# Kernel tuning notes

Measured on AMD Instinct MI355X. Metric: run time of the kernel, lower is better.

The kernel has to match this reference:

```python
import jax, jax.numpy as jnp
import numpy as np

B, N, NPOINT, NSAMPLE, CIN = 8, 16384, 2048, 32, 64
MLP = (64, 64, 128)
EPS = 1e-5  # torch BatchNorm2d default eps


def setup_inputs() -> dict:
    key = jax.random.key(0)
    ks = jax.random.split(key, 8)
    xyz = jax.random.normal(ks[0], (B, 3, N), dtype=jnp.float32)
    points = jax.random.normal(ks[1], (B, CIN, N), dtype=jnp.float32)
    # torch.randperm(N)[:npoint], shared across batch
    sample_idx = jax.random.permutation(ks[2], N)[:NPOINT].astype(jnp.int32)
    c0 = CIN + 3
    def conv_w(k, o, i):
        return jax.random.normal(k, (o, i), dtype=jnp.float32) * np.float32(1.0 / np.sqrt(i))
    W1 = conv_w(ks[3], MLP[0], c0)
    W2 = conv_w(ks[4], MLP[1], MLP[0])
    W3 = conv_w(ks[5], MLP[2], MLP[1])
    return {
        "xyz": xyz, "points": points, "sample_idx": sample_idx,
        "W1": W1, "b1": jnp.zeros((MLP[0],), jnp.float32), "g1": jnp.ones((MLP[0],), jnp.float32), "be1": jnp.zeros((MLP[0],), jnp.float32),
        "W2": W2, "b2": jnp.zeros((MLP[1],), jnp.float32), "g2": jnp.ones((MLP[1],), jnp.float32), "be2": jnp.zeros((MLP[1],), jnp.float32),
        "W3": W3, "b3": jnp.zeros((MLP[2],), jnp.float32), "g3": jnp.ones((MLP[2],), jnp.float32), "be3": jnp.zeros((MLP[2],), jnp.float32),
    }


def _bn(h, g, b):
    # training-mode BatchNorm2d: per-channel (last axis) stats over all other dims, biased var
    m = jnp.mean(h, axis=(0, 1, 2), keepdims=True)
    v = jnp.mean(jnp.square(h - m), axis=(0, 1, 2), keepdims=True)
    return (h - m) * jax.lax.rsqrt(v + EPS) * g + b


def reference(xyz, points, sample_idx, W1, b1, g1, be1, W2, b2, g2, be2, W3, b3, g3, be3):
    # sample npoint centroids (shared indices across batch, as in the torch code)
    q = jnp.take(xyz, sample_idx, axis=2).transpose(0, 2, 1)   # (B, npoint, 3)
    p = xyz.transpose(0, 2, 1)                                  # (B, N, 3)
    # squared pairwise distances (same ordering as cdist for topk)
    d2 = (jnp.sum(q * q, -1)[:, :, None]
          + jnp.sum(p * p, -1)[:, None, :]
          - 2.0 * jnp.einsum('bqc,bnc->bqn', q, p))             # (B, npoint, N)
    _, idx = jax.lax.top_k(-d2, NSAMPLE)                        # (B, npoint, nsample) smallest dists

    gxyz = jnp.take_along_axis(p[:, None, :, :], idx[:, :, :, None], axis=2)  # (B, npoint, nsample, 3)
    rel = gxyz - q[:, :, None, :]
    pf = points.transpose(0, 2, 1)                              # (B, N, C)
    gpts = jnp.take_along_axis(pf[:, None, :, :], idx[:, :, :, None], axis=2)  # (B, npoint, nsample, C)
    feat = jnp.concatenate([rel, gpts], axis=-1)                # (B, npoint, nsample, 3+C)

    h = jax.nn.relu(_bn(jnp.einsum('bpsc,oc->bpso', feat, W1) + b1, g1, be1))
    h = jax.nn.relu(_bn(jnp.einsum('bpsc,oc->bpso', h, W2) + b2, g2, be2))
    h = _bn(jnp.einsum('bpsc,oc->bpso', h, W3) + b3, g3, be3)
    new_points = jnp.max(h, axis=2)                             # max over nsample -> (B, npoint, mlp2)
    return q.transpose(0, 2, 1), new_points.transpose(0, 2, 1)  # (B,3,npoint), (B,mlp2,npoint)
```

## Files before the change

kernel.cpp:

```cpp
#include <hip/hip_runtime.h>
#include <cstdint>

#define DEVFN __device__ __forceinline__

constexpr int B_ = 8, N_ = 16384, NP_ = 2048, NS_ = 32;
constexpr int S_ = B_ * NP_ * NS_;
constexpr float INV_CNT = 1.0f / 524288.0f;

typedef __attribute__((ext_vector_type(8))) short bf8_t;
typedef __attribute__((ext_vector_type(4))) float f4_t;
#define MFMA16(A, Bv, C) __builtin_amdgcn_mfma_f32_16x16x32_bf16(A, Bv, C, 0, 0, 0)

DEVFN unsigned long long wredmin64(unsigned long long v) {
  for (int o = 32; o; o >>= 1) { unsigned long long u = __shfl_xor(v, o); v = u < v ? u : v; }
  return v;
}
DEVFN float d2_ref(float4 q, float4 p) {
  float dot = __fadd_rn(__fadd_rn(__fmul_rn(q.x, p.x), __fmul_rn(q.y, p.y)), __fmul_rn(q.z, p.z));
  return __fsub_rn(__fadd_rn(q.w, p.w), __fadd_rn(dot, dot));
}
DEVFN unsigned int fmono(float d) {
  unsigned int u = __float_as_uint(d);
  return u ^ ((u >> 31) ? 0xFFFFFFFFu : 0x80000000u);
}
DEVFN unsigned short f2bf(float f) {
  unsigned int u = __float_as_uint(f);
  u += 0x7FFFu + ((u >> 16) & 1u);
  return (unsigned short)(u >> 16);
}
DEVFN bf8_t ld_bf8(const unsigned short* p) {
  union { uint4 u; bf8_t b; } cv;
  cv.u = *reinterpret_cast<const uint4*>(p);
  return cv.b;
}

__global__ __launch_bounds__(256) void prep_xyzw(const float* __restrict__ xyz, float4* __restrict__ xyzw) {
  int t = blockIdx.x * 256 + threadIdx.x;
  int b = t >> 14, n = t & (N_ - 1);
  const float* X = xyz + (size_t)b * 3 * N_;
  float x = X[n], y = X[N_ + n], z = X[2 * N_ + n];
  float sq = __fadd_rn(__fadd_rn(__fmul_rn(x, x), __fmul_rn(y, y)), __fmul_rn(z, z));
  xyzw[t] = make_float4(x, y, z, sq);
}

__global__ __launch_bounds__(256) void prep_q(const int* __restrict__ sidx, const float4* __restrict__ xyzw,
                                              float4* __restrict__ qw, float* __restrict__ out_q) {
  int t = blockIdx.x * 256 + threadIdx.x;
  int b = t >> 11, p = t & (NP_ - 1);
  int n = sidx[p] & (N_ - 1);
  float4 v = xyzw[b * N_ + n];
  qw[t] = v;
  out_q[((size_t)b * 3 + 0) * NP_ + p] = v.x;
  out_q[((size_t)b * 3 + 1) * NP_ + p] = v.y;
  out_q[((size_t)b * 3 + 2) * NP_ + p] = v.z;
}

__global__ __launch_bounds__(256) void transpose_bf16(const float* __restrict__ in, unsigned short* __restrict__ out) {
  __shared__ float tile[32][33];
  int b = blockIdx.x >> 10;
  int rem = blockIdx.x & 1023;
  int c0 = (rem >> 9) << 5;
  int n0 = (rem & 511) << 5;
  int tx = threadIdx.x & 31, ty = threadIdx.x >> 5;
#pragma unroll
  for (int jj = 0; jj < 4; jj++) {
    int c = c0 + ty + jj * 8;
    tile[ty + jj * 8][tx] = in[((size_t)b * 64 + c) * N_ + n0 + tx];
  }
  __syncthreads();
#pragma unroll
  for (int jj = 0; jj < 4; jj++) {
    int n = n0 + ty + jj * 8;
    out[((size_t)b * N_ + n) * 64 + c0 + tx] = f2bf(tile[tx][ty + jj * 8]);
  }
}

__global__ __launch_bounds__(256) void prep_w(const float* __restrict__ W1, const float* __restrict__ W2,
                                              const float* __restrict__ W3, unsigned short* __restrict__ W1b,
                                              unsigned short* __restrict__ W2b, unsigned short* __restrict__ W3b) {
  int t = blockIdx.x * 256 + threadIdx.x;
  int stride = gridDim.x * 256;
  for (int e = t; e < 64 * 96; e += stride) {
    int o = e / 96, k = e - o * 96;
    float v = (k < 64) ? W1[o * 67 + 3 + k] : (k < 67 ? W1[o * 67 + (k - 64)] : 0.0f);
    W1b[e] = f2bf(v);
  }
  for (int e = t; e < 64 * 64; e += stride) W2b[e] = f2bf(W2[e]);
  for (int e = t; e < 128 * 64; e += stride) W3b[e] = f2bf(W3[e]);
}

__global__ __launch_bounds__(256) void knn_kernel(const float4* __restrict__ xyzw, const float4* __restrict__ qw,
                                                  int* __restrict__ idx_out) {
  __shared__ unsigned short surv[32][256];
  __shared__ float4 Pst[1024];
  int tid = threadIdx.x;
  int wave = tid >> 6, lane = tid & 63;
  int b = blockIdx.x >> 6;
  int q0 = (blockIdx.x & 63) * 32 + wave * 8;
  const float4* P = xyzw + b * N_;
  float4 Q[8];
#pragma unroll
  for (int j = 0; j < 8; j++) Q[j] = qw[b * NP_ + q0 + j];

  float dmin[8];
#pragma unroll
  for (int j = 0; j < 8; j++) dmin[j] = 1e30f;
  for (int c = 0; c < N_ / 1024; c++) {
    __syncthreads();
#pragma unroll
    for (int u = 0; u < 4; u++) Pst[tid + u * 256] = P[c * 1024 + tid + u * 256];
    __syncthreads();
#pragma unroll 1
    for (int t = 0; t < 16; t++) {
      float4 p = Pst[t * 64 + lane];
      float kx = -2.0f * p.x, ky = -2.0f * p.y, kz = -2.0f * p.z;
#pragma unroll
      for (int j = 0; j < 8; j++) {
        float key = __fmaf_rn(kx, Q[j].x, __fmaf_rn(ky, Q[j].y, __fmaf_rn(kz, Q[j].z, p.w)));
        dmin[j] = fminf(dmin[j], key);
      }
    }
  }
  float T[8];
#pragma unroll 1
  for (int j = 0; j < 8; j++) {
    float v = dmin[j];
#pragma unroll
    for (int k = 2; k <= 64; k <<= 1)
#pragma unroll
      for (int s = k >> 1; s > 0; s >>= 1) {
        float o = __shfl_xor(v, s);
        bool up = ((lane & k) == 0);
        bool tmin = (((lane & s) == 0) == up);
        v = tmin ? fminf(v, o) : fmaxf(v, o);
      }
    T[j] = __shfl(v, 31);
  }
  int base[8];
#pragma unroll
  for (int j = 0; j < 8; j++) base[j] = 0;
  for (int c = 0; c < N_ / 1024; c++) {
    __syncthreads();
#pragma unroll
    for (int u = 0; u < 4; u++) Pst[tid + u * 256] = P[c * 1024 + tid + u * 256];
    __syncthreads();
#pragma unroll 1
    for (int t = 0; t < 16; t++) {
      float4 p = Pst[t * 64 + lane];
      float kx = -2.0f * p.x, ky = -2.0f * p.y, kz = -2.0f * p.z;
#pragma unroll
      for (int j = 0; j < 8; j++) {
        float key = __fmaf_rn(kx, Q[j].x, __fmaf_rn(ky, Q[j].y, __fmaf_rn(kz, Q[j].z, p.w)));
        bool pred = key <= T[j];
        unsigned long long mask = __ballot(pred);
        if (mask) {
          if (pred) {
            int off = base[j] + __popcll(mask & ((1ull << lane) - 1ull));
            if (off < 256) surv[wave * 8 + j][off] = (unsigned short)(c * 1024 + t * 64 + lane);
          }
          base[j] += __popcll(mask);
        }
      }
    }
  }
#pragma unroll 1
  for (int j = 0; j < 8; j++) {
    int qq = wave * 8 + j;
    int m = base[j] < 256 ? base[j] : 256;
    if (m <= 64) {
      unsigned long long v = ~0ull;
      if (lane < m) {
        int n = surv[qq][lane];
        float4 p = P[n];
        float d2 = d2_ref(Q[j], p);
        v = ((unsigned long long)fmono(d2) << 32) | (unsigned int)n;
      }
#pragma unroll
      for (int k = 2; k <= 64; k <<= 1)
#pragma unroll
        for (int s = k >> 1; s > 0; s >>= 1) {
          unsigned long long o = __shfl_xor(v, s);
          bool up = ((lane & k) == 0);
          bool tmin = (((lane & s) == 0) == up);
          unsigned long long lo = v < o ? v : o;
          unsigned long long hi = v < o ? o : v;
          v = tmin ? lo : hi;
        }
      if (lane < 32) idx_out[(b * NP_ + q0 + j) * NS_ + lane] = (int)(v & 0xFFFFu);
    } else {
      unsigned long long k4[4];
#pragma unroll
      for (int t = 0; t < 4; t++) {
        int ii = t * 64 + lane;
        k4[t] = ~0ull;
        if (ii < m) {
          int n = surv[qq][ii];
          float4 p = P[n];
          float d2 = d2_ref(Q[j], p);
          k4[t] = ((unsigned long long)fmono(d2) << 32) | (unsigned int)n;
        }
      }
      int keep = 0;
      for (int r = 0; r < 32; r++) {
        unsigned long long loc = k4[0];
        loc = k4[1] < loc ? k4[1] : loc;
        loc = k4[2] < loc ? k4[2] : loc;
        loc = k4[3] < loc ? k4[3] : loc;
        unsigned long long km = wredmin64(loc);
#pragma unroll
        for (int t = 0; t < 4; t++) if (k4[t] == km) k4[t] = ~0ull;
        if (lane == r) keep = (int)(km & 0xFFFFu);
      }
      if (lane < 32) idx_out[(b * NP_ + q0 + j) * NS_ + lane] = keep;
    }
  }
}

template <int STAGES>
__global__ __launch_bounds__(256, (STAGES == 1) ? 4 : 3) void fused_kernel(
    const int* __restrict__ idx, const float4* __restrict__ xyzw, const float4* __restrict__ qw,
    const unsigned short* __restrict__ pTb, const unsigned short* __restrict__ W1b,
    const unsigned short* __restrict__ W2b, const unsigned short* __restrict__ W3b,
    const float* __restrict__ b1, const float* __restrict__ g1, const float* __restrict__ be1,
    const float* __restrict__ stats1,
    const float* __restrict__ b2, const float* __restrict__ g2, const float* __restrict__ be2,
    const float* __restrict__ stats2,
    const float* __restrict__ b3,
    float* __restrict__ statsOut, float* __restrict__ maxmin) {
  __shared__ unsigned short W1L[64 * 104];
  __shared__ unsigned short W2L[(STAGES >= 2) ? 64 * 72 : 8];
  __shared__ unsigned short W3L[(STAGES == 3) ? 128 * 72 : 8];
  __shared__ unsigned short hbuf[(STAGES >= 2) ? 64 * 64 : 8];
  __shared__ float smx[(STAGES == 3) ? 4 : 1][128];
  __shared__ float smn[(STAGES == 3) ? 4 : 1][128];
  __shared__ float sAcc[256];
  constexpr int NJL = (STAGES == 3) ? 8 : 4;

  int tid = threadIdx.x;
  int w = tid >> 6, l = tid & 63;
  int c16 = l & 15, g = l >> 4;

  for (int e = tid; e < 64 * 12; e += 256) {
    int r = e / 12, c = e % 12;
    *(uint4*)&W1L[r * 104 + c * 8] = *(const uint4*)&W1b[r * 96 + c * 8];
  }
  if (STAGES >= 2)
    for (int e = tid; e < 64 * 8; e += 256) {
      int r = e >> 3, c = e & 7;
      *(uint4*)&W2L[r * 72 + c * 8] = *(const uint4*)&W2b[r * 64 + c * 8];
    }
  if (STAGES == 3)
    for (int e = tid; e < 128 * 8; e += 256) {
      int r = e >> 3, c = e & 7;
      *(uint4*)&W3L[r * 72 + c * 8] = *(const uint4*)&W3b[r * 64 + c * 8];
    }

  float rb1[4], ra1[4], rd1[4], rb2[4], ra2[4], rd2[4], rb3[8];
#pragma unroll
  for (int j = 0; j < 4; j++) rb1[j] = b1[j * 16 + c16];
  if (STAGES >= 2) {
#pragma unroll
    for (int j = 0; j < 4; j++) {
      int ch = j * 16 + c16;
      float m = stats1[ch] * INV_CNT;
      float v = stats1[64 + ch] * INV_CNT - m * m;
      float a = rsqrtf(v + 1e-5f) * g1[ch];
      ra1[j] = a; rd1[j] = be1[ch] - m * a;
      rb2[j] = b2[ch];
    }
  }
  if (STAGES == 3) {
#pragma unroll
    for (int j = 0; j < 4; j++) {
      int ch = j * 16 + c16;
      float m = stats2[ch] * INV_CNT;
      float v = stats2[64 + ch] * INV_CNT - m * m;
      float a = rsqrtf(v + 1e-5f) * g2[ch];
      ra2[j] = a; rd2[j] = be2[ch] - m * a;
    }
#pragma unroll
    for (int j = 0; j < 8; j++) rb3[j] = b3[j * 16 + c16];
  }

  float st1[NJL], st2[NJL];
#pragma unroll
  for (int j = 0; j < NJL; j++) { st1[j] = 0.0f; st2[j] = 0.0f; }

  __syncthreads();

  for (int tile = blockIdx.x; tile < S_ / 64; tile += gridDim.x) {
    int b = tile >> 10;
    int s = tile * 64 + w * 16 + c16;
    int n = idx[s] & (N_ - 1);
    const unsigned short* arow = pTb + (((size_t)(b << 14) + n) << 6);
    bf8_t a0 = ld_bf8(arow + g * 8);
    bf8_t a1 = ld_bf8(arow + 32 + g * 8);
    float4 P = xyzw[(b << 14) + n];
    float4 Q = qw[tile * 2 + (w >> 1)];
    bf8_t a2 = {0, 0, 0, 0, 0, 0, 0, 0};
    if (g == 0) {
      a2[0] = (short)f2bf(P.x - Q.x);
      a2[1] = (short)f2bf(P.y - Q.y);
      a2[2] = (short)f2bf(P.z - Q.z);
    }
    f4_t acc1[4];
#pragma unroll
    for (int j = 0; j < 4; j++) {
      bf8_t w0 = ld_bf8(&W1L[(j * 16 + c16) * 104 + 0 * 32 + g * 8]);
      bf8_t w1 = ld_bf8(&W1L[(j * 16 + c16) * 104 + 1 * 32 + g * 8]);
      bf8_t w2 = ld_bf8(&W1L[(j * 16 + c16) * 104 + 2 * 32 + g * 8]);
      acc1[j] = (f4_t){0.0f, 0.0f, 0.0f, 0.0f};
      acc1[j] = MFMA16(a0, w0, acc1[j]);
      acc1[j] = MFMA16(a1, w1, acc1[j]);
      acc1[j] = MFMA16(a2, w2, acc1[j]);
    }
    if (STAGES == 1) {
#pragma unroll
      for (int j = 0; j < 4; j++)
#pragma unroll
        for (int r = 0; r < 4; r++) {
          float h = acc1[j][r] + rb1[j];
          st1[j] += h; st2[j] += h * h;
        }
      continue;
    }
    if (STAGES == 2) __syncthreads();
#pragma unroll
    for (int j = 0; j < 4; j++)
#pragma unroll
      for (int r = 0; r < 4; r++) {
        float h = acc1[j][r] + rb1[j];
        float t = fmaxf(0.0f, fmaf(h, ra1[j], rd1[j]));
        int row = w * 16 + g * 4 + r, ch = j * 16 + c16;
        hbuf[row * 64 + (((ch >> 3) ^ (row & 7)) << 3) + (ch & 7)] = f2bf(t);
      }
    __syncthreads();
    int rrow = w * 16 + c16;
    bf8_t h1f[2];
#pragma unroll
    for (int kb = 0; kb < 2; kb++)
      h1f[kb] = ld_bf8(hbuf + rrow * 64 + (((kb * 4 + g) ^ (rrow & 7)) << 3));
    f4_t acc2[4];
#pragma unroll
    for (int j = 0; j < 4; j++) {
      bf8_t w0 = ld_bf8(&W2L[(j * 16 + c16) * 72 + g * 8]);
      bf8_t w1 = ld_bf8(&W2L[(j * 16 + c16) * 72 + 32 + g * 8]);
      acc2[j] = (f4_t){0.0f, 0.0f, 0.0f, 0.0f};
      acc2[j] = MFMA16(h1f[0], w0, acc2[j]);
      acc2[j] = MFMA16(h1f[1], w1, acc2[j]);
    }
    if (STAGES == 2) {
#pragma unroll
      for (int j = 0; j < 4; j++)
#pragma unroll
        for (int r = 0; r < 4; r++) {
          float h = acc2[j][r] + rb2[j];
          st1[j] += h; st2[j] += h * h;
        }
      continue;
    }
    __syncthreads();
#pragma unroll
    for (int j = 0; j < 4; j++)
#pragma unroll
      for (int r = 0; r < 4; r++) {
        float h = acc2[j][r] + rb2[j];
        float t = fmaxf(0.0f, fmaf(h, ra2[j], rd2[j]));
        int row = w * 16 + g * 4 + r, ch = j * 16 + c16;
        hbuf[row * 64 + (((ch >> 3) ^ (row & 7)) << 3) + (ch & 7)] = f2bf(t);
      }
    __syncthreads();
    bf8_t h2f[2];
#pragma unroll
    for (int kb = 0; kb < 2; kb++)
      h2f[kb] = ld_bf8(hbuf + rrow * 64 + (((kb * 4 + g) ^ (rrow & 7)) << 3));
    f4_t acc3[8];
#pragma unroll
    for (int j = 0; j < 8; j++) {
      bf8_t w0 = ld_bf8(&W3L[(j * 16 + c16) * 72 + g * 8]);
      bf8_t w1 = ld_bf8(&W3L[(j * 16 + c16) * 72 + 32 + g * 8]);
      acc3[j] = (f4_t){0.0f, 0.0f, 0.0f, 0.0f};
      acc3[j] = MFMA16(h2f[0], w0, acc3[j]);
      acc3[j] = MFMA16(h2f[1], w1, acc3[j]);
    }
    float mx[8], mn[8];
#pragma unroll
    for (int j = 0; j < 8; j++) {
      mx[j] = -1e30f; mn[j] = 1e30f;
#pragma unroll
      for (int r = 0; r < 4; r++) {
        float h = acc3[j][r] + rb3[j];
        st1[j] += h; st2[j] += h * h;
        mx[j] = fmaxf(mx[j], h); mn[j] = fminf(mn[j], h);
      }
      mx[j] = fmaxf(mx[j], __shfl_xor(mx[j], 16));
      mx[j] = fmaxf(mx[j], __shfl_xor(mx[j], 32));
      mn[j] = fminf(mn[j], __shfl_xor(mn[j], 16));
      mn[j] = fminf(mn[j], __shfl_xor(mn[j], 32));
    }
    if (l < 16) {
#pragma unroll
      for (int j = 0; j < 8; j++) { smx[w][j * 16 + l] = mx[j]; smn[w][j * 16 + l] = mn[j]; }
    }
    __syncthreads();
    {
      int cen = tid >> 7, ch = tid & 127;
      float vx = fmaxf(smx[2 * cen][ch], smx[2 * cen + 1][ch]);
      float vn = fminf(smn[2 * cen][ch], smn[2 * cen + 1][ch]);
      size_t gcen = (size_t)tile * 2 + cen;
      maxmin[gcen * 256 + ch * 2 + 0] = vx;
      maxmin[gcen * 256 + ch * 2 + 1] = vn;
    }
  }
  __syncthreads();
  if (tid < 2 * NJL * 16) sAcc[tid] = 0.0f;
  __syncthreads();
#pragma unroll
  for (int j = 0; j < NJL; j++) {
    atomicAdd(&sAcc[j * 16 + c16], st1[j]);
    atomicAdd(&sAcc[NJL * 16 + j * 16 + c16], st2[j]);
  }
  __syncthreads();
  if (tid < 2 * NJL * 16) atomicAdd(&statsOut[tid], sAcc[tid]);
}

__global__ __launch_bounds__(256) void finalize_kernel(const float* __restrict__ maxmin,
                                                       const float* __restrict__ stats3,
                                                       const float* __restrict__ g3, const float* __restrict__ be3,
                                                       float* __restrict__ out_np) {
  int o = blockIdx.x * 256 + threadIdx.x;
  int p = o & 2047, ch = (o >> 11) & 127, b = o >> 18;
  float m = stats3[ch] * INV_CNT;
  float v = stats3[128 + ch] * INV_CNT - m * m;
  float a = rsqrtf(v + 1e-5f) * g3[ch];
  float d = be3[ch] - m * a;
  size_t g = (size_t)(b * 2048 + p);
  float hi = maxmin[g * 256 + ch * 2 + 0];
  float lo = maxmin[g * 256 + ch * 2 + 1];
  out_np[o] = fmaf(a, (a >= 0.0f ? hi : lo), d);
}

extern "C" void kernel_launch(void* const* d_in, const int* in_sizes, int n_in,
                              void* d_out, int out_size, void* d_ws, size_t ws_size,
                              hipStream_t stream) {
  const float* xyz = (const float*)d_in[0];
  const float* points = (const float*)d_in[1];
  const int* sidx = (const int*)d_in[2];
  const float* W1 = (const float*)d_in[3];
  const float* b1 = (const float*)d_in[4];
  const float* g1 = (const float*)d_in[5];
  const float* be1 = (const float*)d_in[6];
  const float* W2 = (const float*)d_in[7];
  const float* b2 = (const float*)d_in[8];
  const float* g2 = (const float*)d_in[9];
  const float* be2 = (const float*)d_in[10];
  const float* W3 = (const float*)d_in[11];
  const float* b3 = (const float*)d_in[12];
  const float* g3 = (const float*)d_in[13];
  const float* be3 = (const float*)d_in[14];

  float* out_q = (float*)d_out;
  float* out_np = (float*)d_out + (size_t)B_ * 3 * NP_;

  char* ws = (char*)d_ws;
  float* stats1 = (float*)(ws + 0);
  float* stats2 = (float*)(ws + 512);
  float* stats3 = (float*)(ws + 1024);
  size_t off = 4096;
  float4* xyzw = (float4*)(ws + off); off += (size_t)B_ * N_ * 16;
  float4* qw = (float4*)(ws + off);   off += (size_t)B_ * NP_ * 16;
  int* idxb = (int*)(ws + off);       off += (size_t)B_ * NP_ * NS_ * 4;
  unsigned short* pTb = (unsigned short*)(ws + off); off += (size_t)B_ * N_ * 64 * 2;
  unsigned short* W1b = (unsigned short*)(ws + off); off += 64 * 96 * 2;
  unsigned short* W2b = (unsigned short*)(ws + off); off += 64 * 64 * 2;
  unsigned short* W3b = (unsigned short*)(ws + off); off += 128 * 64 * 2;
  float* maxmin = (float*)(ws + off);  off += (size_t)B_ * NP_ * 128 * 2 * 4;

  hipMemsetAsync(ws, 0, 4096, stream);
  prep_xyzw<<<B_ * N_ / 256, 256, 0, stream>>>(xyz, xyzw);
  prep_q<<<B_ * NP_ / 256, 256, 0, stream>>>(sidx, xyzw, qw, out_q);
  transpose_bf16<<<B_ * 2 * (N_ / 32), 256, 0, stream>>>(points, pTb);
  prep_w<<<72, 256, 0, stream>>>(W1, W2, W3, W1b, W2b, W3b);
  knn_kernel<<<B_ * (NP_ / 32), 256, 0, stream>>>(xyzw, qw, idxb);
  fused_kernel<1><<<1024, 256, 0, stream>>>(idxb, xyzw, qw, pTb, W1b, W2b, W3b,
      b1, g1, be1, stats1, b2, g2, be2, stats2, b3, stats1, maxmin);
  fused_kernel<2><<<1024, 256, 0, stream>>>(idxb, xyzw, qw, pTb, W1b, W2b, W3b,
      b1, g1, be1, stats1, b2, g2, be2, stats2, b3, stats2, maxmin);
  fused_kernel<3><<<1024, 256, 0, stream>>>(idxb, xyzw, qw, pTb, W1b, W2b, W3b,
      b1, g1, be1, stats1, b2, g2, be2, stats2, b3, stats3, maxmin);
  finalize_kernel<<<(B_ * 128 * NP_) / 256, 256, 0, stream>>>(maxmin, stats3, g3, be3, out_np);
}
```

Before: 483.8 us.

## Materialize MLP activations in bf16 and restructure kNN to split points across waves

The recompute scheme, where each BN stage re-runs every earlier layer, is replaced by three kernels that write pre-BN activations as bf16 to a workspace buffer and read them back for the next layer. BN and ReLU are applied when the data is loaded. This trades about 64 MB of global traffic per stage for the repeated layer-1/layer-2 matmuls and gathers. The kNN kernel now gives each block 16 queries, with each wave scanning a quarter of the points for all 16 queries. Survivor counts are merged through shared-memory atomics, which adds atomic and sync overhead but reduces the per-wave point loop. The new path runs only when the workspace is large enough, and the old path stays as a fallback.

```diff
diff --git a/kernel.cpp b/kernel.cpp
--- a/kernel.cpp
+++ b/kernel.cpp
@@ -10,6 +10,8 @@
 typedef __attribute__((ext_vector_type(8))) short bf8_t;
 typedef __attribute__((ext_vector_type(4))) float f4_t;
 #define MFMA16(A, Bv, C) __builtin_amdgcn_mfma_f32_16x16x32_bf16(A, Bv, C, 0, 0, 0)
+
+union u4s8 { uint4 u; unsigned short s[8]; };
 
 DEVFN unsigned long long wredmin64(unsigned long long v) {
   for (int o = 32; o; o >>= 1) { unsigned long long u = __shfl_xor(v, o); v = u < v ? u : v; }
@@ -89,42 +91,53 @@
   for (int e = t; e < 128 * 64; e += stride) W3b[e] = f2bf(W3[e]);
 }
 
-__global__ __launch_bounds__(256) void knn_kernel(const float4* __restrict__ xyzw, const float4* __restrict__ qw,
-                                                  int* __restrict__ idx_out) {
-  __shared__ unsigned short surv[32][256];
+__global__ __launch_bounds__(256, 4) void knn_kernel(const float4* __restrict__ xyzw,
+                                                     const float4* __restrict__ qw,
+                                                     int* __restrict__ idx_out) {
   __shared__ float4 Pst[1024];
-  int tid = threadIdx.x;
-  int wave = tid >> 6, lane = tid & 63;
-  int b = blockIdx.x >> 6;
-  int q0 = (blockIdx.x & 63) * 32 + wave * 8;
+  __shared__ unsigned short surv[16][256];
+  __shared__ float Tsh[16];
+  __shared__ int cnt[16];
+  int tid = threadIdx.x, wave = tid >> 6, lane = tid & 63;
+  int b = blockIdx.x >> 7;
+  int q0 = (blockIdx.x & 127) * 16;
   const float4* P = xyzw + b * N_;
-  float4 Q[8];
-#pragma unroll
-  for (int j = 0; j < 8; j++) Q[j] = qw[b * NP_ + q0 + j];
-
-  float dmin[8];
-#pragma unroll
-  for (int j = 0; j < 8; j++) dmin[j] = 1e30f;
+  float Qx[16], Qy[16], Qz[16];
+#pragma unroll
+  for (int j = 0; j < 16; j++) {
+    float4 q = qw[b * NP_ + q0 + j];
+    Qx[j] = q.x; Qy[j] = q.y; Qz[j] = q.z;
+  }
+  float dmin[16];
+#pragma unroll
+  for (int j = 0; j < 16; j++) dmin[j] = 1e30f;
   for (int c = 0; c < N_ / 1024; c++) {
     __syncthreads();
 #pragma unroll
     for (int u = 0; u < 4; u++) Pst[tid + u * 256] = P[c * 1024 + tid + u * 256];
     __syncthreads();
+#pragma unroll
+    for (int t = 0; t < 4; t++) {
+      float4 p = Pst[wave * 256 + t * 64 + lane];
+      float kx = -2.0f * p.x, ky = -2.0f * p.y, kz = -2.0f * p.z;
+#pragma unroll
+      for (int j = 0; j < 16; j++) {
+        float key = __fmaf_rn(kx, Qx[j], __fmaf_rn(ky, Qy[j], __fmaf_rn(kz, Qz[j], p.w)));
+        dmin[j] = fminf(dmin[j], key);
+      }
+    }
+  }
+  __syncthreads();
+  float* dl = (float*)Pst;
+#pragma unroll
+  for (int j = 0; j < 16; j++) dl[j * 256 + wave * 64 + lane] = dmin[j];
+  if (tid < 16) cnt[tid] = 0;
+  __syncthreads();
 #pragma unroll 1
-    for (int t = 0; t < 16; t++) {
-      float4 p = Pst[t * 64 + lane];
-      float kx = -2.0f * p.x, ky = -2.0f * p.y, kz = -2.0f * p.z;
-#pragma unroll
-      for (int j = 0; j < 8; j++) {
-        float key = __fmaf_rn(kx, Q[j].x, __fmaf_rn(ky, Q[j].y, __fmaf_rn(kz, Q[j].z, p.w)));
-        dmin[j] = fminf(dmin[j], key);
-      }
-    }
-  }
-  float T[8];
-#pragma unroll 1
-  for (int j = 0; j < 8; j++) {
-    float v = dmin[j];
+  for (int jj = 0; jj < 4; jj++) {
+    int j = wave * 4 + jj;
+    float v = fminf(fminf(dl[j * 256 + lane], dl[j * 256 + 64 + lane]),
+                    fminf(dl[j * 256 + 128 + lane], dl[j * 256 + 192 + lane]));
 #pragma unroll
     for (int k = 2; k <= 64; k <<= 1)
 #pragma unroll
@@ -134,45 +147,51 @@
         bool tmin = (((lane & s) == 0) == up);
         v = tmin ? fminf(v, o) : fmaxf(v, o);
       }
-    T[j] = __shfl(v, 31);
-  }
-  int base[8];
-#pragma unroll
-  for (int j = 0; j < 8; j++) base[j] = 0;
+    if (lane == 31) Tsh[j] = v;
+  }
+  __syncthreads();
+  float T[16];
+#pragma unroll
+  for (int j = 0; j < 16; j++) T[j] = Tsh[j];
   for (int c = 0; c < N_ / 1024; c++) {
     __syncthreads();
 #pragma unroll
     for (int u = 0; u < 4; u++) Pst[tid + u * 256] = P[c * 1024 + tid + u * 256];
     __syncthreads();
 #pragma unroll 1
-    for (int t = 0; t < 16; t++) {
-      float4 p = Pst[t * 64 + lane];
+    for (int t = 0; t < 4; t++) {
+      int n = c * 1024 + wave * 256 + t * 64 + lane;
+      float4 p = Pst[wave * 256 + t * 64 + lane];
       float kx = -2.0f * p.x, ky = -2.0f * p.y, kz = -2.0f * p.z;
 #pragma unroll
-      for (int j = 0; j < 8; j++) {
-        float key = __fmaf_rn(kx, Q[j].x, __fmaf_rn(ky, Q[j].y, __fmaf_rn(kz, Q[j].z, p.w)));
+      for (int j = 0; j < 16; j++) {
+        float key = __fmaf_rn(kx, Qx[j], __fmaf_rn(ky, Qy[j], __fmaf_rn(kz, Qz[j], p.w)));
         bool pred = key <= T[j];
         unsigned long long mask = __ballot(pred);
         if (mask) {
+          int basew;
+          if (lane == 0) basew = atomicAdd(&cnt[j], (int)__popcll(mask));
+          basew = __shfl(basew, 0);
           if (pred) {
-            int off = base[j] + __popcll(mask & ((1ull << lane) - 1ull));
-            if (off < 256) surv[wave * 8 + j][off] = (unsigned short)(c * 1024 + t * 64 + lane);
+            int off = basew + (int)__popcll(mask & ((1ull << lane) - 1ull));
+            if (off < 256) surv[j][off] = (unsigned short)n;
           }
-          base[j] += __popcll(mask);
         }
       }
     }
   }
+  __syncthreads();
 #pragma unroll 1
-  for (int j = 0; j < 8; j++) {
-    int qq = wave * 8 + j;
-    int m = base[j] < 256 ? base[j] : 256;
+  for (int jj = 0; jj < 4; jj++) {
+    int j = wave * 4 + jj;
+    float4 Q = qw[b * NP_ + q0 + j];
+    int m = cnt[j] < 256 ? cnt[j] : 256;
     if (m <= 64) {
       unsigned long long v = ~0ull;
       if (lane < m) {
-        int n = surv[qq][lane];
+        int n = surv[j][lane];
         float4 p = P[n];
-        float d2 = d2_ref(Q[j], p);
+        float d2 = d2_ref(Q, p);
         v = ((unsigned long long)fmono(d2) << 32) | (unsigned int)n;
       }
 #pragma unroll
@@ -194,9 +213,9 @@
         int ii = t * 64 + lane;
         k4[t] = ~0ull;
         if (ii < m) {
-          int n = surv[qq][ii];
+          int n = surv[j][ii];
           float4 p = P[n];
-          float d2 = d2_ref(Q[j], p);
+          float d2 = d2_ref(Q, p);
           k4[t] = ((unsigned long long)fmono(d2) << 32) | (unsigned int)n;
         }
       }
@@ -214,6 +233,255 @@
       if (lane < 32) idx_out[(b * NP_ + q0 + j) * NS_ + lane] = keep;
     }
   }
+}
+
+
+__global__ __launch_bounds__(256, 4) void fused1_mat(
+    const int* __restrict__ idx, const float4* __restrict__ xyzw, const float4* __restrict__ qw,
+    const unsigned short* __restrict__ pTb, const unsigned short* __restrict__ W1b,
+    const float* __restrict__ b1, float* __restrict__ statsOut, unsigned short* __restrict__ h) {
+  __shared__ unsigned short W1L[64 * 104];
+  __shared__ unsigned short hbuf[64 * 64];
+  __shared__ float sAcc[128];
+  int tid = threadIdx.x;
+  int w = tid >> 6, l = tid & 63;
+  int c16 = l & 15, g = l >> 4;
+  for (int e = tid; e < 64 * 12; e += 256) {
+    int r = e / 12, c = e % 12;
+    *(uint4*)&W1L[r * 104 + c * 8] = *(const uint4*)&W1b[r * 96 + c * 8];
+  }
+  float rb1[4];
+#pragma unroll
+  for (int j = 0; j < 4; j++) rb1[j] = b1[j * 16 + c16];
+  float st1[4] = {0, 0, 0, 0}, st2[4] = {0, 0, 0, 0};
+  __syncthreads();
+  for (int tile = blockIdx.x; tile < S_ / 64; tile += gridDim.x) {
+    int b = tile >> 10;
+    int s = tile * 64 + w * 16 + c16;
+    int n = idx[s] & (N_ - 1);
+    const unsigned short* arow = pTb + (((size_t)(b << 14) + n) << 6);
+    bf8_t a0 = ld_bf8(arow + g * 8);
+    bf8_t a1 = ld_bf8(arow + 32 + g * 8);
+    float4 P = xyzw[(b << 14) + n];
+    float4 Q = qw[tile * 2 + (w >> 1)];
+    bf8_t a2 = {0, 0, 0, 0, 0, 0, 0, 0};
+    if (g == 0) {
+      a2[0] = (short)f2bf(P.x - Q.x);
+      a2[1] = (short)f2bf(P.y - Q.y);
+      a2[2] = (short)f2bf(P.z - Q.z);
+    }
+    f4_t acc1[4];
+#pragma unroll
+    for (int j = 0; j < 4; j++) {
+      bf8_t w0 = ld_bf8(&W1L[(j * 16 + c16) * 104 + 0 * 32 + g * 8]);
+      bf8_t w1 = ld_bf8(&W1L[(j * 16 + c16) * 104 + 1 * 32 + g * 8]);
+      bf8_t w2 = ld_bf8(&W1L[(j * 16 + c16) * 104 + 2 * 32 + g * 8]);
+      acc1[j] = (f4_t){0.0f, 0.0f, 0.0f, 0.0f};
+      acc1[j] = MFMA16(a0, w0, acc1[j]);
+      acc1[j] = MFMA16(a1, w1, acc1[j]);
+      acc1[j] = MFMA16(a2, w2, acc1[j]);
+    }
+    __syncthreads();
+#pragma unroll
+    for (int j = 0; j < 4; j++)
+#pragma unroll
+      for (int r = 0; r < 4; r++) {
+        float hv = acc1[j][r] + rb1[j];
+        st1[j] += hv; st2[j] += hv * hv;
+        int row = w * 16 + g * 4 + r, ch = j * 16 + c16;
+        hbuf[row * 64 + (((ch >> 3) ^ (row & 7)) << 3) + (ch & 7)] = f2bf(hv);
+      }
+    __syncthreads();
+    int rrow = w * 16 + c16;
+    uint4 v0 = *(const uint4*)&hbuf[rrow * 64 + ((g ^ (rrow & 7)) << 3)];
+    uint4 v1 = *(const uint4*)&hbuf[rrow * 64 + (((4 + g) ^ (rrow & 7)) << 3)];
+    uint4* hd = (uint4*)(h + (((size_t)tile * 64 + rrow) << 6));
+    hd[g] = v0;
+    hd[4 + g] = v1;
+  }
+  __syncthreads();
+  if (tid < 128) sAcc[tid] = 0.0f;
+  __syncthreads();
+#pragma unroll
+  for (int j = 0; j < 4; j++) {
+    atomicAdd(&sAcc[j * 16 + c16], st1[j]);
+    atomicAdd(&sAcc[64 + j * 16 + c16], st2[j]);
+  }
+  __syncthreads();
+  if (tid < 128) atomicAdd(&statsOut[tid], sAcc[tid]);
+}
+
+__global__ __launch_bounds__(256, 4) void fused2_mat(
+    const unsigned short* __restrict__ W2b, const float* __restrict__ g1, const float* __restrict__ be1,
+    const float* __restrict__ stats1, const float* __restrict__ b2,
+    float* __restrict__ statsOut, unsigned short* __restrict__ h) {
+  __shared__ unsigned short W2L[64 * 72];
+  __shared__ unsigned short hbuf[64 * 64];
+  __shared__ float sa1[64], sd1[64];
+  __shared__ float sAcc[128];
+  int tid = threadIdx.x;
+  int w = tid >> 6, l = tid & 63;
+  int c16 = l & 15, g = l >> 4;
+  for (int e = tid; e < 64 * 8; e += 256) {
+    int r = e >> 3, c = e & 7;
+    *(uint4*)&W2L[r * 72 + c * 8] = *(const uint4*)&W2b[r * 64 + c * 8];
+  }
+  if (tid < 64) {
+    float m = stats1[tid] * INV_CNT;
+    float v = stats1[64 + tid] * INV_CNT - m * m;
+    float a = rsqrtf(v + 1e-5f) * g1[tid];
+    sa1[tid] = a;
+    sd1[tid] = be1[tid] - m * a;
+  }
+  float rb2[4];
+#pragma unroll
+  for (int j = 0; j < 4; j++) rb2[j] = b2[j * 16 + c16];
+  float st1[4] = {0, 0, 0, 0}, st2[4] = {0, 0, 0, 0};
+  __syncthreads();
+  for (int tile = blockIdx.x; tile < S_ / 64; tile += gridDim.x) {
+    int rrow = w * 16 + c16;
+    uint4* hd = (uint4*)(h + (((size_t)tile * 64 + rrow) << 6));
+    u4s8 c0, c1;
+    c0.u = hd[g];
+    c1.u = hd[4 + g];
+    bf8_t a0f, a1f;
+#pragma unroll
+    for (int e = 0; e < 8; e++) {
+      float x0 = __uint_as_float((unsigned)c0.s[e] << 16);
+      float x1 = __uint_as_float((unsigned)c1.s[e] << 16);
+      a0f[e] = (short)f2bf(fmaxf(0.0f, fmaf(x0, sa1[g * 8 + e], sd1[g * 8 + e])));
+      a1f[e] = (short)f2bf(fmaxf(0.0f, fmaf(x1, sa1[32 + g * 8 + e], sd1[32 + g * 8 + e])));
+    }
+    f4_t acc2[4];
+#pragma unroll
+    for (int j = 0; j < 4; j++) {
+      bf8_t w0 = ld_bf8(&W2L[(j * 16 + c16) * 72 + g * 8]);
+      bf8_t w1 = ld_bf8(&W2L[(j * 16 + c16) * 72 + 32 + g * 8]);
+      acc2[j] = (f4_t){0.0f, 0.0f, 0.0f, 0.0f};
+      acc2[j] = MFMA16(a0f, w0, acc2[j]);
+      acc2[j] = MFMA16(a1f, w1, acc2[j]);
+    }
+    __syncthreads();
+#pragma unroll
+    for (int j = 0; j < 4; j++)
+#pragma unroll
+      for (int r = 0; r < 4; r++) {
+        float hv = acc2[j][r] + rb2[j];
+        st1[j] += hv; st2[j] += hv * hv;
+        int row = w * 16 + g * 4 + r, ch = j * 16 + c16;
+        hbuf[row * 64 + (((ch >> 3) ^ (row & 7)) << 3) + (ch & 7)] = f2bf(hv);
+      }
+    __syncthreads();
+    uint4 v0 = *(const uint4*)&hbuf[rrow * 64 + ((g ^ (rrow & 7)) << 3)];
+    uint4 v1 = *(const uint4*)&hbuf[rrow * 64 + (((4 + g) ^ (rrow & 7)) << 3)];
+    hd[g] = v0;
+    hd[4 + g] = v1;
+  }
+  __syncthreads();
+  if (tid < 128) sAcc[tid] = 0.0f;
+  __syncthreads();
+#pragma unroll
+  for (int j = 0; j < 4; j++) {
+    atomicAdd(&sAcc[j * 16 + c16], st1[j]);
+    atomicAdd(&sAcc[64 + j * 16 + c16], st2[j]);
+  }
+  __syncthreads();
+  if (tid < 128) atomicAdd(&statsOut[tid], sAcc[tid]);
+}
+
+__global__ __launch_bounds__(256, 4) void fused3_mat(
+    const unsigned short* __restrict__ W3b, const float* __restrict__ g2, const float* __restrict__ be2,
+    const float* __restrict__ stats2, const float* __restrict__ b3,
+    float* __restrict__ statsOut, const unsigned short* __restrict__ h, float* __restrict__ maxmin) {
+  __shared__ unsigned short W3L[128 * 72];
+  __shared__ float sa2[64], sd2[64];
+  __shared__ float smx[4][128];
+  __shared__ float smn[4][128];
+  __shared__ float sAcc[256];
+  int tid = threadIdx.x;
+  int w = tid >> 6, l = tid & 63;
+  int c16 = l & 15, g = l >> 4;
+  for (int e = tid; e < 128 * 8; e += 256) {
+    int r = e >> 3, c = e & 7;
+    *(uint4*)&W3L[r * 72 + c * 8] = *(const uint4*)&W3b[r * 64 + c * 8];
+  }
+  if (tid < 64) {
+    float m = stats2[tid] * INV_CNT;
+    float v = stats2[64 + tid] * INV_CNT - m * m;
+    float a = rsqrtf(v + 1e-5f) * g2[tid];
+    sa2[tid] = a;
+    sd2[tid] = be2[tid] - m * a;
+  }
+  float rb3[8];
+#pragma unroll
+  for (int j = 0; j < 8; j++) rb3[j] = b3[j * 16 + c16];
+  float st1[8], st2[8];
+#pragma unroll
+  for (int j = 0; j < 8; j++) { st1[j] = 0.0f; st2[j] = 0.0f; }
+  __syncthreads();
+  for (int tile = blockIdx.x; tile < S_ / 64; tile += gridDim.x) {
+    int rrow = w * 16 + c16;
+    const uint4* hd = (const uint4*)(h + (((size_t)tile * 64 + rrow) << 6));
+    u4s8 c0, c1;
+    c0.u = hd[g];
+    c1.u = hd[4 + g];
+    bf8_t a0f, a1f;
+#pragma unroll
+    for (int e = 0; e < 8; e++) {
+      float x0 = __uint_as_float((unsigned)c0.s[e] << 16);
+      float x1 = __uint_as_float((unsigned)c1.s[e] << 16);
+      a0f[e] = (short)f2bf(fmaxf(0.0f, fmaf(x0, sa2[g * 8 + e], sd2[g * 8 + e])));
+      a1f[e] = (short)f2bf(fmaxf(0.0f, fmaf(x1, sa2[32 + g * 8 + e], sd2[32 + g * 8 + e])));
+    }
+    f4_t acc3[8];
+#pragma unroll
+    for (int j = 0; j < 8; j++) {
+      bf8_t w0 = ld_bf8(&W3L[(j * 16 + c16) * 72 + g * 8]);
+      bf8_t w1 = ld_bf8(&W3L[(j * 16 + c16) * 72 + 32 + g * 8]);
+      acc3[j] = (f4_t){0.0f, 0.0f, 0.0f, 0.0f};
+      acc3[j] = MFMA16(a0f, w0, acc3[j]);
+      acc3[j] = MFMA16(a1f, w1, acc3[j]);
+    }
+    float mx[8], mn[8];
+#pragma unroll
+    for (int j = 0; j < 8; j++) {
+      mx[j] = -1e30f; mn[j] = 1e30f;
+#pragma unroll
+      for (int r = 0; r < 4; r++) {
+        float hv = acc3[j][r] + rb3[j];
+        st1[j] += hv; st2[j] += hv * hv;
+        mx[j] = fmaxf(mx[j], hv); mn[j] = fminf(mn[j], hv);
+      }
+      mx[j] = fmaxf(mx[j], __shfl_xor(mx[j], 16));
+      mx[j] = fmaxf(mx[j], __shfl_xor(mx[j], 32));
+      mn[j] = fminf(mn[j], __shfl_xor(mn[j], 16));
+      mn[j] = fminf(mn[j], __shfl_xor(mn[j], 32));
+    }
+    __syncthreads();
+    if (l < 16) {
+#pragma unroll
+      for (int j = 0; j < 8; j++) { smx[w][j * 16 + l] = mx[j]; smn[w][j * 16 + l] = mn[j]; }
+    }
+    __syncthreads();
+    {
+      int cen = tid >> 7, ch = tid & 127;
+      float vx = fmaxf(smx[2 * cen][ch], smx[2 * cen + 1][ch]);
+      float vn = fminf(smn[2 * cen][ch], smn[2 * cen + 1][ch]);
+      size_t gcen = (size_t)tile * 2 + cen;
+      maxmin[gcen * 256 + ch * 2 + 0] = vx;
+      maxmin[gcen * 256 + ch * 2 + 1] = vn;
+    }
+  }
+  __syncthreads();
+  if (tid < 256) sAcc[tid] = 0.0f;
+  __syncthreads();
+#pragma unroll
+  for (int j = 0; j < 8; j++) {
+    atomicAdd(&sAcc[j * 16 + c16], st1[j]);
+    atomicAdd(&sAcc[128 + j * 16 + c16], st2[j]);
+  }
+  __syncthreads();
+  if (tid < 256) atomicAdd(&statsOut[tid], sAcc[tid]);
 }
 
 template <int STAGES>
@@ -235,11 +503,9 @@
   __shared__ float smn[(STAGES == 3) ? 4 : 1][128];
   __shared__ float sAcc[256];
   constexpr int NJL = (STAGES == 3) ? 8 : 4;
-
   int tid = threadIdx.x;
   int w = tid >> 6, l = tid & 63;
   int c16 = l & 15, g = l >> 4;
-
   for (int e = tid; e < 64 * 12; e += 256) {
     int r = e / 12, c = e % 12;
     *(uint4*)&W1L[r * 104 + c * 8] = *(const uint4*)&W1b[r * 96 + c * 8];
@@ -254,7 +520,6 @@
       int r = e >> 3, c = e & 7;
       *(uint4*)&W3L[r * 72 + c * 8] = *(const uint4*)&W3b[r * 64 + c * 8];
     }
-
   float rb1[4], ra1[4], rd1[4], rb2[4], ra2[4], rd2[4], rb3[8];
 #pragma unroll
   for (int j = 0; j < 4; j++) rb1[j] = b1[j * 16 + c16];
@@ -281,13 +546,10 @@
 #pragma unroll
     for (int j = 0; j < 8; j++) rb3[j] = b3[j * 16 + c16];
   }
-
   float st1[NJL], st2[NJL];
 #pragma unroll
   for (int j = 0; j < NJL; j++) { st1[j] = 0.0f; st2[j] = 0.0f; }
-
-  __syncthreads();
-
+  __syncthreads();
   for (int tile = blockIdx.x; tile < S_ / 64; tile += gridDim.x) {
     int b = tile >> 10;
     int s = tile * 64 + w * 16 + c16;
@@ -319,8 +581,8 @@
       for (int j = 0; j < 4; j++)
 #pragma unroll
         for (int r = 0; r < 4; r++) {
-          float h = acc1[j][r] + rb1[j];
-          st1[j] += h; st2[j] += h * h;
+          float hv = acc1[j][r] + rb1[j];
+          st1[j] += hv; st2[j] += hv * hv;
         }
       continue;
     }
@@ -329,8 +591,8 @@
     for (int j = 0; j < 4; j++)
 #pragma unroll
       for (int r = 0; r < 4; r++) {
-        float h = acc1[j][r] + rb1[j];
-        float t = fmaxf(0.0f, fmaf(h, ra1[j], rd1[j]));
+        float hv = acc1[j][r] + rb1[j];
+        float t = fmaxf(0.0f, fmaf(hv, ra1[j], rd1[j]));
         int row = w * 16 + g * 4 + r, ch = j * 16 + c16;
         hbuf[row * 64 + (((ch >> 3) ^ (row & 7)) << 3) + (ch & 7)] = f2bf(t);
       }
@@ -354,8 +616,8 @@
       for (int j = 0; j < 4; j++)
 #pragma unroll
         for (int r = 0; r < 4; r++) {
-          float h = acc2[j][r] + rb2[j];
-          st1[j] += h; st2[j] += h * h;
+          float hv = acc2[j][r] + rb2[j];
+          st1[j] += hv; st2[j] += hv * hv;
         }
       continue;
     }
@@ -364,8 +626,8 @@
     for (int j = 0; j < 4; j++)
 #pragma unroll
       for (int r = 0; r < 4; r++) {
-        float h = acc2[j][r] + rb2[j];
-        float t = fmaxf(0.0f, fmaf(h, ra2[j], rd2[j]));
+        float hv = acc2[j][r] + rb2[j];
+        float t = fmaxf(0.0f, fmaf(hv, ra2[j], rd2[j]));
         int row = w * 16 + g * 4 + r, ch = j * 16 + c16;
         hbuf[row * 64 + (((ch >> 3) ^ (row & 7)) << 3) + (ch & 7)] = f2bf(t);
       }
@@ -389,9 +651,9 @@
       mx[j] = -1e30f; mn[j] = 1e30f;
 #pragma unroll
       for (int r = 0; r < 4; r++) {
-        float h = acc3[j][r] + rb3[j];
-        st1[j] += h; st2[j] += h * h;
-        mx[j] = fmaxf(mx[j], h); mn[j] = fminf(mn[j], h);
+        float hv = acc3[j][r] + rb3[j];
+        st1[j] += hv; st2[j] += hv * hv;
+        mx[j] = fmaxf(mx[j], hv); mn[j] = fminf(mn[j], hv);
       }
       mx[j] = fmaxf(mx[j], __shfl_xor(mx[j], 16));
       mx[j] = fmaxf(mx[j], __shfl_xor(mx[j], 32));
@@ -475,18 +737,26 @@
   unsigned short* W2b = (unsigned short*)(ws + off); off += 64 * 64 * 2;
   unsigned short* W3b = (unsigned short*)(ws + off); off += 128 * 64 * 2;
   float* maxmin = (float*)(ws + off);  off += (size_t)B_ * NP_ * 128 * 2 * 4;
+  unsigned short* hG = (unsigned short*)(ws + off); off += (size_t)S_ * 64 * 2;
+  bool use_mat = (ws_size >= off);
 
   hipMemsetAsync(ws, 0, 4096, stream);
   prep_xyzw<<<B_ * N_ / 256, 256, 0, stream>>>(xyz, xyzw);
   prep_q<<<B_ * NP_ / 256, 256, 0, stream>>>(sidx, xyzw, qw, out_q);
   transpose_bf16<<<B_ * 2 * (N_ / 32), 256, 0, stream>>>(points, pTb);
   prep_w<<<72, 256, 0, stream>>>(W1, W2, W3, W1b, W2b, W3b);
-  knn_kernel<<<B_ * (NP_ / 32), 256, 0, stream>>>(xyzw, qw, idxb);
-  fused_kernel<1><<<1024, 256, 0, stream>>>(idxb, xyzw, qw, pTb, W1b, W2b, W3b,
-      b1, g1, be1, stats1, b2, g2, be2, stats2, b3, stats1, maxmin);
-  fused_kernel<2><<<1024, 256, 0, stream>>>(idxb, xyzw, qw, pTb, W1b, W2b, W3b,
-      b1, g1, be1, stats1, b2, g2, be2, stats2, b3, stats2, maxmin);
-  fused_kernel<3><<<1024, 256, 0, stream>>>(idxb, xyzw, qw, pTb, W1b, W2b, W3b,
-      b1, g1, be1, stats1, b2, g2, be2, stats2, b3, stats3, maxmin);
+  knn_kernel<<<B_ * (NP_ / 16), 256, 0, stream>>>(xyzw, qw, idxb);
+  if (use_mat) {
+    fused1_mat<<<1024, 256, 0, stream>>>(idxb, xyzw, qw, pTb, W1b, b1, stats1, hG);
+    fused2_mat<<<1024, 256, 0, stream>>>(W2b, g1, be1, stats1, b2, stats2, hG);
+    fused3_mat<<<1024, 256, 0, stream>>>(W3b, g2, be2, stats2, b3, stats3, hG, maxmin);
+  } else {
+    fused_kernel<1><<<1024, 256, 0, stream>>>(idxb, xyzw, qw, pTb, W1b, W2b, W3b,
+        b1, g1, be1, stats1, b2, g2, be2, stats2, b3, stats1, maxmin);
+    fused_kernel<2><<<1024, 256, 0, stream>>>(idxb, xyzw, qw, pTb, W1b, W2b, W3b,
+        b1, g1, be1, stats1, b2, g2, be2, stats2, b3, stats2, maxmin);
+    fused_kernel<3><<<1024, 256, 0, stream>>>(idxb, xyzw, qw, pTb, W1b, W2b, W3b,
+        b1, g1, be1, stats1, b2, g2, be2, stats2, b3, stats3, maxmin);
+  }
   finalize_kernel<<<(B_ * 128 * NP_) / 256, 256, 0, stream>>>(maxmin, stats3, g3, be3, out_np);
 }
```

Measured after the change: 403.6 us. -16.6%, faster.
